# Optimization experiments

Hardware: AMD Instinct MI355X
Metric: run time of the kernel (lower is better)

Reference implementation:

```python
import jax, jax.numpy as jnp
import numpy as np

B, SW, SE, D, H, FF = 8, 512, 128, 1024, 16, 4096
HD = D // H
EPS = 1e-12
SCALE = 1.0 / np.sqrt(HD).astype(np.float32)


def _split_heads(x):
    # [B, S, D] -> [B, H, S, HD]
    b, s, _ = x.shape
    return x.reshape(b, s, H, HD).transpose(0, 2, 1, 3)


def _layer_norm(x, g, b):
    m = jnp.mean(x, axis=-1, keepdims=True)
    v = jnp.mean(jnp.square(x - m), axis=-1, keepdims=True)
    return g * (x - m) / jnp.sqrt(v + EPS) + b


def setup_inputs() -> dict:
    key = jax.random.key(0)
    ks = iter(jax.random.split(key, 40))
    std = 0.02

    def w(i, o):
        return jax.random.normal(next(ks), (i, o), jnp.float32) * std

    inp = {
        "word_hidden_states": jax.random.normal(next(ks), (B, SW, D), jnp.float32),
        "entity_hidden_states": jax.random.normal(next(ks), (B, SE, D), jnp.float32),
        "word_attention_mask": jnp.zeros((B, SW), jnp.float32),
        "entity_attention_mask": jnp.zeros((B, SE), jnp.float32),
        # entity-aware self attention projections
        "Wq": w(D, D), "bq": jnp.zeros((D,), jnp.float32),
        "Ww2e": w(D, D), "bw2e": jnp.zeros((D,), jnp.float32),
        "We2w": w(D, D), "be2w": jnp.zeros((D,), jnp.float32),
        "We2e": w(D, D), "be2e": jnp.zeros((D,), jnp.float32),
        "Wk": w(D, D), "bk": jnp.zeros((D,), jnp.float32),
        "Wv": w(D, D), "bv": jnp.zeros((D,), jnp.float32),
        # BertSelfOutput
        "Wo": w(D, D), "bo": jnp.zeros((D,), jnp.float32),
        "ln1_g": jnp.ones((D,), jnp.float32), "ln1_b": jnp.zeros((D,), jnp.float32),
        # BertIntermediate / BertOutput
        "Wi": w(D, FF), "bi": jnp.zeros((FF,), jnp.float32),
        "Wout": w(FF, D), "bout": jnp.zeros((D,), jnp.float32),
        "ln2_g": jnp.ones((D,), jnp.float32), "ln2_b": jnp.zeros((D,), jnp.float32),
    }
    return inp


def _layer(wh, eh, wmask, emask, Wq, bq, Ww2e, bw2e, We2w, be2w, We2e, be2e,
           Wk, bk, Wv, bv, Wo, bo, ln1_g, ln1_b, Wi, bi, Wout, bout, ln2_g, ln2_b):
    sw = wh.shape[1]
    hidden = jnp.concatenate([wh, eh], axis=1)              # [B, S, D]
    mask = jnp.concatenate([wmask, emask], axis=-1)[:, None, None, :]  # additive

    q_w2w = _split_heads(wh @ Wq + bq)
    q_w2e = _split_heads(wh @ Ww2e + bw2e)
    q_e2w = _split_heads(eh @ We2w + be2w)
    q_e2e = _split_heads(eh @ We2e + be2e)
    k = _split_heads(hidden @ Wk + bk)                      # [B, H, S, HD]
    kw, ke = k[:, :, :sw, :], k[:, :, sw:, :]

    s_w2w = jnp.einsum("bhqd,bhkd->bhqk", q_w2w, kw)
    s_w2e = jnp.einsum("bhqd,bhkd->bhqk", q_w2e, ke)
    s_e2w = jnp.einsum("bhqd,bhkd->bhqk", q_e2w, kw)
    s_e2e = jnp.einsum("bhqd,bhkd->bhqk", q_e2e, ke)
    word_scores = jnp.concatenate([s_w2w, s_w2e], axis=3)
    ent_scores = jnp.concatenate([s_e2w, s_e2e], axis=3)
    scores = jnp.concatenate([word_scores, ent_scores], axis=2) * SCALE + mask
    probs = jax.nn.softmax(scores, axis=-1)

    v = _split_heads(hidden @ Wv + bv)
    ctx = jnp.einsum("bhqk,bhkd->bhqd", probs, v)
    ctx = ctx.transpose(0, 2, 1, 3).reshape(wh.shape[0], -1, D)  # [B, S, D]

    # BertSelfOutput: dense + residual + LN
    attn_out = _layer_norm(ctx @ Wo + bo + hidden, ln1_g, ln1_b)
    # BertIntermediate + BertOutput
    inter = jax.nn.gelu(attn_out @ Wi + bi, approximate=False)
    out = _layer_norm(inter @ Wout + bout + attn_out, ln2_g, ln2_b)
    return out[:, :sw, :], out[:, sw:, :]


def reference(word_hidden_states, entity_hidden_states, word_attention_mask,
              entity_attention_mask, Wq, bq, Ww2e, bw2e, We2w, be2w, We2e, be2e,
              Wk, bk, Wv, bv, Wo, bo, ln1_g, ln1_b, Wi, bi, Wout, bout,
              ln2_g, ln2_b):
    return _layer(word_hidden_states, entity_hidden_states, word_attention_mask,
                  entity_attention_mask, Wq, bq, Ww2e, bw2e, We2w, be2w, We2e,
                  be2e, Wk, bk, Wv, bv, Wo, bo, ln1_g, ln1_b, Wi, bi, Wout,
                  bout, ln2_g, ln2_b)
```

## Files before the change

kernel.cpp:

```cpp
#include <hip/hip_runtime.h>
#include <hip/hip_bf16.h>
#include <stdint.h>
#include <math.h>

#define DEV __device__ __forceinline__

using bf16 = __hip_bfloat16;
typedef __attribute__((ext_vector_type(8))) short bf16x8;
typedef __attribute__((ext_vector_type(4))) float f32x4;

static constexpr int NB  = 8;
static constexpr int NSW = 512;
static constexpr int NSE = 128;
static constexpr int ND  = 1024;
static constexpr int NH  = 16;
static constexpr int NFF = 4096;
static constexpr int NS  = NSW + NSE;
static constexpr int NHD = 64;

DEV f32x4 mfma16(bf16x8 a, bf16x8 b, f32x4 c){
  return __builtin_amdgcn_mfma_f32_16x16x32_bf16(a, b, c, 0, 0, 0);
}

DEV void gload16(const bf16* g, bf16* l){
  __builtin_amdgcn_global_load_lds((const __attribute__((address_space(1))) void*)g,
                                   (__attribute__((address_space(3))) void*)l,
                                   16, 0, 0);
}

DEV bf16 tobf(float f){ return __float2bfloat16(f); }

union PK4 { bf16 h[4]; short4 s; };

__global__ __launch_bounds__(256) void cast_word_k(const float* __restrict__ wh,
                                                   bf16* __restrict__ hid){
  long i = ((long)blockIdx.x*256 + threadIdx.x)*4;
  float4 v = *reinterpret_cast<const float4*>(wh + i);
  PK4 p; p.h[0]=tobf(v.x); p.h[1]=tobf(v.y); p.h[2]=tobf(v.z); p.h[3]=tobf(v.w);
  long row = i >> 10; int c = (int)(i & 1023);
  int b = (int)(row >> 9), s = (int)(row & 511);
  *reinterpret_cast<short4*>(hid + ((long)(b*NS + s) << 10) + c) = p.s;
}

__global__ __launch_bounds__(256) void cast_ent_k(const float* __restrict__ eh,
                                                  bf16* __restrict__ hid){
  long i = ((long)blockIdx.x*256 + threadIdx.x)*4;
  float4 v = *reinterpret_cast<const float4*>(eh + i);
  PK4 p; p.h[0]=tobf(v.x); p.h[1]=tobf(v.y); p.h[2]=tobf(v.z); p.h[3]=tobf(v.w);
  long row = i >> 10; int c = (int)(i & 1023);
  int b = (int)(row >> 7), s = (int)(row & 127);
  *reinterpret_cast<short4*>(hid + ((long)(b*NS + NSW + s) << 10) + c) = p.s;
}

struct TP7 { const float* src[7]; bf16* dst[7]; };

__global__ void transpose7_k(TP7 tp){
  __shared__ float tile[32][33];
  const float* in = tp.src[blockIdx.z];
  bf16* out = tp.dst[blockIdx.z];
  const int c0 = blockIdx.x*32, r0 = blockIdx.y*32;
  const int tx = threadIdx.x, ty = threadIdx.y;
  #pragma unroll
  for (int i=0;i<4;i++)
    tile[ty + i*8][tx] = in[(long)(r0 + ty + i*8)*1024 + c0 + tx];
  __syncthreads();
  #pragma unroll
  for (int i=0;i<4;i++){
    int rr = ty + i*8;
    out[(long)(c0 + rr)*1024 + r0 + tx] = tobf(tile[tx][rr]);
  }
}

__global__ void transpose_cast_k(const float* __restrict__ in, bf16* __restrict__ out,
                                 int R, int C){
  __shared__ float tile[32][33];
  const int c0 = blockIdx.x*32, r0 = blockIdx.y*32;
  const int tx = threadIdx.x, ty = threadIdx.y;
  #pragma unroll
  for (int i=0;i<4;i++)
    tile[ty + i*8][tx] = in[(long)(r0 + ty + i*8)*C + c0 + tx];
  __syncthreads();
  #pragma unroll
  for (int i=0;i<4;i++){
    int rr = ty + i*8;
    out[(long)(c0 + rr)*R + r0 + tx] = tobf(tile[tx][rr]);
  }
}

__global__ void bias_concat_k(const float* __restrict__ bq, const float* __restrict__ bw2e,
                              const float* __restrict__ be2w, const float* __restrict__ be2e,
                              const float* __restrict__ bk, const float* __restrict__ bv,
                              float* __restrict__ bQw, float* __restrict__ bQe,
                              float* __restrict__ bKV){
  int i = blockIdx.x*256 + threadIdx.x;
  bQw[i] = bq[i];   bQw[1024+i] = bw2e[i];
  bQe[i] = be2w[i]; bQe[1024+i] = be2e[i];
  bKV[i] = bk[i];   bKV[1024+i] = bv[i];
}

template<int NF>
DEV void stA(bf16* reg, const bf16* a0, const bf16* a1, int koff, int tid){
  gload16(a0 + koff, reg + tid*8);
  gload16(a1 + koff, reg + (512 + tid)*8);
}
template<int NF>
DEV void stB(bf16* reg, const bf16* b0, const bf16* b1, int koff, int tid){
  gload16(b0 + koff, reg + tid*8);
  if constexpr (NF == 4) gload16(b1 + koff, reg + (512 + tid)*8);
}

template<int NF>
DEV void g256_core(const bf16* a0, const bf16* a1,
                   const bf16* b0, const bf16* b1,
                   int NT, bf16* lds, f32x4 (&acc)[8][NF],
                   int tid, int wr, int wc, int lane){
  constexpr int AKH  = 8192;
  constexpr int BKH  = NF*2048;
  constexpr int BUFE = 2*AKH + 2*BKH;
  auto Areg = [&](int buf,int kh){ return lds + buf*BUFE + kh*AKH; };
  auto Breg = [&](int buf,int kh){ return lds + buf*BUFE + 2*AKH + kh*BKH; };
  auto gate = [&](bool last){
    if (last){
      asm volatile("s_waitcnt vmcnt(0)" ::: "memory");
    } else if constexpr (NF == 4){
      asm volatile("s_waitcnt vmcnt(4)" ::: "memory");
    } else {
      asm volatile("s_waitcnt vmcnt(3)" ::: "memory");
    }
    __builtin_amdgcn_sched_barrier(0);
    asm volatile("s_barrier" ::: "memory");
    __builtin_amdgcn_sched_barrier(0);
  };
  stA<NF>(Areg(0,0), a0, a1, 0,  tid);
  stB<NF>(Breg(0,0), b0, b1, 0,  tid);
  stA<NF>(Areg(0,1), a0, a1, 32, tid);
  stB<NF>(Breg(0,1), b0, b1, 32, tid);
  int kt = 0;
  for (int t=0; t<NT; ++t){
    const int c = t & 1;
    const bool more = (t+1 < NT);
    const int kn = kt + 64;
    #pragma unroll
    for (int ks=0; ks<2; ++ks){
      gate(!more && ks==1);
      if (more) stA<NF>(Areg(c^1, ks), a0, a1, kn + ks*32, tid);
      const bf16* Ar = Areg(c, ks);
      const bf16* Br = Breg(c, ks);
      bf16x8 bfr[NF], afr[4];
      #pragma unroll
      for (int nf=0; nf<NF; ++nf)
        bfr[nf] = *reinterpret_cast<const bf16x8*>(Br + (((wc*NF+nf)<<6) + lane)*8);
      #pragma unroll
      for (int m=0; m<4; ++m)
        afr[m] = *reinterpret_cast<const bf16x8*>(Ar + (((wr*8+m)<<6) + lane)*8);
      __builtin_amdgcn_s_setprio(1);
      #pragma unroll
      for (int m=0; m<4; ++m)
        #pragma unroll
        for (int nf=0; nf<NF; ++nf)
          acc[m][nf] = mfma16(afr[m], bfr[nf], acc[m][nf]);
      __builtin_amdgcn_s_setprio(0);
      if (more) stB<NF>(Breg(c^1, ks), b0, b1, kn + ks*32, tid);
      #pragma unroll
      for (int m=0; m<4; ++m)
        afr[m] = *reinterpret_cast<const bf16x8*>(Ar + (((wr*8+4+m)<<6) + lane)*8);
      __builtin_amdgcn_s_setprio(1);
      #pragma unroll
      for (int m=0; m<4; ++m)
        #pragma unroll
        for (int nf=0; nf<NF; ++nf)
          acc[4+m][nf] = mfma16(afr[m], bfr[nf], acc[4+m][nf]);
      __builtin_amdgcn_s_setprio(0);
    }
    kt = kn;
  }
}

__global__ __launch_bounds__(512, 2) void proj_k(const bf16* __restrict__ hid,
    const bf16* __restrict__ WqwT, const bf16* __restrict__ WqeT,
    const bf16* __restrict__ WkvT,
    const float* __restrict__ bQw, const float* __restrict__ bQe,
    const float* __restrict__ bKV,
    bf16* __restrict__ Qwb, bf16* __restrict__ Qeb,
    bf16* __restrict__ KVb, bf16* __restrict__ Vt){
  __shared__ __align__(16) bf16 lds[2*(2*8192 + 2*8192)];
  const int tid = threadIdx.x, wid = tid>>6, lane = tid&63;
  const int wr = wid>>2, wc = wid&3, lr = lane&15, lg = lane>>4;
  int wg = blockIdx.x;
  { int xcd = wg & 7, idx = wg >> 3; wg = xcd*40 + idx; }
  const bool isKV = (wg >= 160);
  const int loc = isKV ? wg - 160 : wg;
  const int m0 = (loc >> 3)*256, n0 = (loc & 7)*256;
  const bool word = (m0 < 4096);

  const int la = lane & 15, ksub = (lane>>4)*8;
  auto hidrow = [&](int r)->long{
    if (isKV) return r;
    if (word) return (long)((r>>9)*640 + (r&511));
    int r2 = r - 4096; return (long)((r2>>7)*640 + 512 + (r2&127));
  };
  const bf16* a0 = hid + hidrow(m0 + wid*16 + la)*1024 + ksub;
  const bf16* a1 = hid + hidrow(m0 + (wid+8)*16 + la)*1024 + ksub;
  const bf16* Bt = isKV ? WkvT : (word ? WqwT : WqeT);
  const bf16* b0 = Bt + (long)(n0 + wid*16 + la)*1024 + ksub;
  const bf16* b1 = Bt + (long)(n0 + (wid+8)*16 + la)*1024 + ksub;

  f32x4 acc[8][4];
  #pragma unroll
  for (int m=0;m<8;m++)
    #pragma unroll
    for (int n=0;n<4;n++) acc[m][n] = (f32x4){0.f,0.f,0.f,0.f};

  g256_core<4>(a0, a1, b0, b1, 16, lds, acc, tid, wr, wc, lane);

  const float* bias = isKV ? bKV : (word ? bQw : bQe);
  #pragma unroll
  for (int m=0;m<8;m++){
    const int rbase = m0 + wr*128 + m*16 + lg*4;
    #pragma unroll
    for (int nf=0;nf<4;nf++){
      const int col = n0 + wc*64 + nf*16 + lr;
      const float bsv = bias[col];
      #pragma unroll
      for (int r=0;r<4;r++){
        const int rw = rbase + r;
        const float v = acc[m][nf][r] + bsv;
        if (!isKV){
          if (word) Qwb[(long)rw*2048 + col] = tobf(v);
          else      Qeb[(long)(rw-4096)*2048 + col] = tobf(v);
        } else {
          if (col < 1024){
            KVb[(long)rw*2048 + col] = tobf(v);
          } else {
            int b = rw / NS, s = rw % NS, hh = (col-1024)>>6, dd = (col-1024)&63;
            Vt[((long)((b*NH + hh)*NHD + dd))*NS + s] = tobf(v);
          }
        }
      }
    }
  }
}

__global__ __launch_bounds__(512, 2) void ffn1_k(const bf16* __restrict__ A,
    const bf16* __restrict__ Bt, const float* __restrict__ bias,
    bf16* __restrict__ out){
  __shared__ __align__(16) bf16 lds[2*(2*8192 + 2*8192)];
  const int tid = threadIdx.x, wid = tid>>6, lane = tid&63;
  const int wr = wid>>2, wc = wid&3, lr = lane&15, lg = lane>>4;
  int wg = blockIdx.x;
  { int xcd = wg & 7, idx = wg >> 3; wg = xcd*40 + idx; }
  const int m0 = (wg >> 4)*256, n0 = (wg & 15)*256;

  const int la = lane & 15, ksub = (lane>>4)*8;
  const bf16* a0 = A + (long)(m0 + wid*16 + la)*1024 + ksub;
  const bf16* a1 = A + (long)(m0 + (wid+8)*16 + la)*1024 + ksub;
  const bf16* b0 = Bt + (long)(n0 + wid*16 + la)*1024 + ksub;
  const bf16* b1 = Bt + (long)(n0 + (wid+8)*16 + la)*1024 + ksub;

  f32x4 acc[8][4];
  #pragma unroll
  for (int m=0;m<8;m++)
    #pragma unroll
    for (int n=0;n<4;n++) acc[m][n] = (f32x4){0.f,0.f,0.f,0.f};

  g256_core<4>(a0, a1, b0, b1, 16, lds, acc, tid, wr, wc, lane);

  #pragma unroll
  for (int m=0;m<8;m++){
    const int rbase = m0 + wr*128 + m*16 + lg*4;
    #pragma unroll
    for (int nf=0;nf<4;nf++){
      const int col = n0 + wc*64 + nf*16 + lr;
      const float bsv = bias[col];
      #pragma unroll
      for (int r=0;r<4;r++){
        float v = acc[m][nf][r] + bsv;
        float ge = 0.5f*v*(1.0f + erff(v*0.70710678118654752f));
        out[(long)(rbase+r)*NFF + col] = tobf(ge);
      }
    }
  }
}

__global__ __launch_bounds__(512, 2) void ws_k(const bf16* __restrict__ A, int lda,
    const bf16* __restrict__ Bt, const float* __restrict__ bias,
    float* __restrict__ out0, float* __restrict__ out1, int Kc){
  __shared__ __align__(16) bf16 lds[2*(2*8192 + 2*4096)];
  const int tid = threadIdx.x, wid = tid>>6, lane = tid&63;
  const int wr = wid>>2, wc = wid&3, lr = lane&15, lg = lane>>4;
  int wg = blockIdx.x;
  { int xcd = wg & 7, idx = wg >> 3; wg = xcd*20 + idx; }
  const int m0 = (wg >> 3)*256, n0 = (wg & 7)*128;
  const int kt0 = blockIdx.z * Kc;

  const int la = lane & 15, ksub = (lane>>4)*8;
  const bf16* a0 = A + (long)(m0 + wid*16 + la)*lda + kt0 + ksub;
  const bf16* a1 = A + (long)(m0 + (wid+8)*16 + la)*lda + kt0 + ksub;
  const bf16* b0 = Bt + (long)(n0 + wid*16 + la)*lda + kt0 + ksub;

  f32x4 acc[8][2];
  #pragma unroll
  for (int m=0;m<8;m++)
    #pragma unroll
    for (int n=0;n<2;n++) acc[m][n] = (f32x4){0.f,0.f,0.f,0.f};

  g256_core<2>(a0, a1, b0, b0, Kc/64, lds, acc, tid, wr, wc, lane);

  float* out = blockIdx.z ? out1 : out0;
  #pragma unroll
  for (int m=0;m<8;m++){
    const int rbase = m0 + wr*128 + m*16 + lg*4;
    #pragma unroll
    for (int nf=0;nf<2;nf++){
      const int col = n0 + wc*32 + nf*16 + lr;
      const float bsv = blockIdx.z ? 0.f : bias[col];
      #pragma unroll
      for (int r=0;r<4;r++)
        out[(long)(rbase+r)*1024 + col] = acc[m][nf][r] + bsv;
    }
  }
}

__global__ __launch_bounds__(256) void attn_k(
    const bf16* __restrict__ Qw, const bf16* __restrict__ Qe,
    const bf16* __restrict__ KV, const bf16* __restrict__ Vt,
    const float* __restrict__ wm, const float* __restrict__ em,
    bf16* __restrict__ ctx){
  __shared__ __align__(16) bf16 Plds[4][2][16*40];
  __shared__ float mred[4][2][16];
  __shared__ float lred[4][2][16];
  __shared__ __align__(16) float accred[4][16][64];
  const int tid = threadIdx.x, wid = tid>>6, lane = tid&63;
  const int lr = lane&15, lg = lane>>4;
  const int w   = blockIdx.x;
  const int b   = w / (NH*20);
  const int rem = w % (NH*20);
  const int h   = rem / 20;
  const int q0  = (rem % 20)*32;

  const bf16* Qbase; long qrow0;
  if (q0 < NSW){ Qbase = Qw; qrow0 = (long)b*NSW + q0; }
  else         { Qbase = Qe; qrow0 = (long)b*NSE + (q0 - NSW); }

  bf16x8 qA[2][2], qB[2][2];
  #pragma unroll
  for (int m=0;m<2;m++)
    #pragma unroll
    for (int dc=0; dc<2; dc++){
      long o = (qrow0 + m*16 + lr)*2048 + h*NHD + dc*32 + lg*8;
      qA[m][dc] = *reinterpret_cast<const bf16x8*>(Qbase + o);
      qB[m][dc] = *reinterpret_cast<const bf16x8*>(Qbase + o + 1024);
    }

  const f32x4 zero = {0.f,0.f,0.f,0.f};
  f32x4 cacc[2][4];
  float mrow[2][4], lsum[2][4];
  #pragma unroll
  for (int m=0;m<2;m++){
    #pragma unroll
    for (int dt=0;dt<4;dt++) cacc[m][dt] = zero;
    #pragma unroll
    for (int r=0;r<4;r++){ mrow[m][r] = -1e30f; lsum[m][r] = 0.f; }
  }

  const bf16* Kbase = KV + (long)b*NS*2048 + h*NHD;
  const bf16* Vbase = Vt + (long)((b*NH + h)*NHD)*NS;

  for (int kt=wid*5; kt<wid*5+5; kt++){
    const int k0 = kt*32;
    const bool word = (k0 < NSW);

    bf16x8 kf[2][2], vf[4];
    #pragma unroll
    for (int sub=0;sub<2;sub++)
      #pragma unroll
      for (int dc=0;dc<2;dc++)
        kf[sub][dc] = *reinterpret_cast<const bf16x8*>(
            Kbase + (long)(k0 + sub*16 + lr)*2048 + dc*32 + lg*8);
    #pragma unroll
    for (int dt=0;dt<4;dt++)
      vf[dt] = *reinterpret_cast<const bf16x8*>(
          Vbase + (long)(dt*16 + lr)*NS + k0 + lg*8);

    float msk0, msk1;
    { int k = k0 + lr;
      msk0 = word ? wm[b*NSW + k]      : em[b*NSE + (k - NSW)];
      msk1 = word ? wm[b*NSW + k + 16] : em[b*NSE + (k + 16 - NSW)];
    }

    f32x4 sc[2][2];
    #pragma unroll
    for (int m=0;m<2;m++){ sc[m][0]=zero; sc[m][1]=zero; }
    __builtin_amdgcn_s_setprio(1);
    #pragma unroll
    for (int m=0;m<2;m++)
      #pragma unroll
      for (int sub=0;sub<2;sub++)
        #pragma unroll
        for (int dc=0;dc<2;dc++){
          const bf16x8 q = word ? qA[m][dc] : qB[m][dc];
          sc[m][sub] = mfma16(q, kf[sub][dc], sc[m][sub]);
        }
    __builtin_amdgcn_s_setprio(0);

    #pragma unroll
    for (int m=0;m<2;m++){
      bf16* pw = &Plds[wid][m][0];
      #pragma unroll
      for (int r=0;r<4;r++){
        float s0 = sc[m][0][r]*0.125f + msk0;
        float s1 = sc[m][1][r]*0.125f + msk1;
        float t = fmaxf(s0, s1);
        #pragma unroll
        for (int o=8;o;o>>=1) t = fmaxf(t, __shfl_xor(t, o, 16));
        float mn = fmaxf(mrow[m][r], t);
        float al = __expf(mrow[m][r] - mn);
        mrow[m][r] = mn;
        float p0 = __expf(s0 - mn), p1 = __expf(s1 - mn);
        float ps = p0 + p1;
        #pragma unroll
        for (int o=8;o;o>>=1) ps += __shfl_xor(ps, o, 16);
        lsum[m][r] = lsum[m][r]*al + ps;
        pw[(lg*4+r)*40 + lr]      = tobf(p0);
        pw[(lg*4+r)*40 + 16 + lr] = tobf(p1);
        #pragma unroll
        for (int dt=0;dt<4;dt++) cacc[m][dt][r] *= al;
      }
    }

    __builtin_amdgcn_s_setprio(1);
    #pragma unroll
    for (int m=0;m<2;m++){
      bf16x8 pa = *reinterpret_cast<const bf16x8*>(&Plds[wid][m][0] + lr*40 + lg*8);
      #pragma unroll
      for (int dt=0;dt<4;dt++)
        cacc[m][dt] = mfma16(pa, vf[dt], cacc[m][dt]);
    }
    __builtin_amdgcn_s_setprio(0);
  }

  #pragma unroll
  for (int m=0;m<2;m++)
    #pragma unroll
    for (int r=0;r<4;r++)
      if (lr == 0){
        mred[wid][m][lg*4+r] = mrow[m][r];
        lred[wid][m][lg*4+r] = lsum[m][r];
      }
  __syncthreads();

  float Lg[2][4], scl[2][4];
  #pragma unroll
  for (int m=0;m<2;m++)
    #pragma unroll
    for (int r=0;r<4;r++){
      const int row = lg*4 + r;
      float M0 = fmaxf(fmaxf(mred[0][m][row], mred[1][m][row]),
                       fmaxf(mred[2][m][row], mred[3][m][row]));
      float lt = 0.f;
      #pragma unroll
      for (int ww=0; ww<4; ww++)
        lt += lred[ww][m][row] * __expf(mred[ww][m][row] - M0);
      Lg[m][r]  = lt;
      scl[m][r] = __expf(mrow[m][r] - M0);
    }

  const long crow = (long)b*NS + q0;
  #pragma unroll
  for (int m=0;m<2;m++){
    #pragma unroll
    for (int dt=0;dt<4;dt++)
      #pragma unroll
      for (int r=0;r<4;r++)
        accred[wid][dt*4+r][lane] = cacc[m][dt][r] * scl[m][r];
    __syncthreads();
    { const int dt = wid;
      #pragma unroll
      for (int r=0;r<4;r++){
        float s = accred[0][dt*4+r][lane] + accred[1][dt*4+r][lane]
                + accred[2][dt*4+r][lane] + accred[3][dt*4+r][lane];
        s /= Lg[m][r];
        ctx[(crow + m*16 + lg*4 + r)*ND + h*NHD + dt*16 + lr] = tobf(s);
      }
    }
    __syncthreads();
  }
}

DEV void block_red2(float& s1, float& s2){
  __shared__ float red[8];
  #pragma unroll
  for (int o=32;o;o>>=1){ s1 += __shfl_down(s1,o); s2 += __shfl_down(s2,o); }
  int wid = threadIdx.x>>6, lane = threadIdx.x&63;
  if (lane==0){ red[wid]=s1; red[4+wid]=s2; }
  __syncthreads();
  s1 = red[0]+red[1]+red[2]+red[3];
  s2 = red[4]+red[5]+red[6]+red[7];
}

__global__ __launch_bounds__(256) void ln1_k(const float* __restrict__ ctxO,
    const float* __restrict__ ctxO1,
    const float* __restrict__ wh, const float* __restrict__ eh,
    const float* __restrict__ g, const float* __restrict__ be,
    float* __restrict__ outF, bf16* __restrict__ outB){
  const int row = blockIdx.x;
  const int b = row / NS, s = row % NS;
  const float* resid = (s < NSW) ? wh + ((long)(b*NSW + s))*ND
                                 : eh + ((long)(b*NSE + (s-NSW)))*ND;
  const int t = threadIdx.x;
  float4 xv = reinterpret_cast<const float4*>(ctxO + (long)row*ND)[t];
  float4 x1 = reinterpret_cast<const float4*>(ctxO1 + (long)row*ND)[t];
  float4 rv = reinterpret_cast<const float4*>(resid)[t];
  float4 x = make_float4(xv.x+x1.x+rv.x, xv.y+x1.y+rv.y, xv.z+x1.z+rv.z, xv.w+x1.w+rv.w);
  float s1 = x.x+x.y+x.z+x.w;
  float s2 = x.x*x.x + x.y*x.y + x.z*x.z + x.w*x.w;
  block_red2(s1, s2);
  float mean = s1 * (1.f/ND);
  float var  = s2 * (1.f/ND) - mean*mean;
  float rstd = rsqrtf(var + 1e-12f);
  float4 gv = reinterpret_cast<const float4*>(g)[t];
  float4 bv = reinterpret_cast<const float4*>(be)[t];
  float4 y = make_float4(gv.x*(x.x-mean)*rstd + bv.x,
                         gv.y*(x.y-mean)*rstd + bv.y,
                         gv.z*(x.z-mean)*rstd + bv.z,
                         gv.w*(x.w-mean)*rstd + bv.w);
  reinterpret_cast<float4*>(outF + (long)row*ND)[t] = y;
  PK4 p; p.h[0]=tobf(y.x); p.h[1]=tobf(y.y); p.h[2]=tobf(y.z); p.h[3]=tobf(y.w);
  reinterpret_cast<short4*>(outB + (long)row*ND)[t] = p.s;
}

__global__ __launch_bounds__(256) void ln2_k(const float* __restrict__ ffo,
    const float* __restrict__ ffo1,
    const float* __restrict__ attnF, const float* __restrict__ g,
    const float* __restrict__ be, float* __restrict__ out){
  const int row = blockIdx.x;
  const int b = row / NS, s = row % NS;
  const int t = threadIdx.x;
  float4 xv = reinterpret_cast<const float4*>(ffo + (long)row*ND)[t];
  float4 x1 = reinterpret_cast<const float4*>(ffo1 + (long)row*ND)[t];
  float4 rv = reinterpret_cast<const float4*>(attnF + (long)row*ND)[t];
  float4 x = make_float4(xv.x+x1.x+rv.x, xv.y+x1.y+rv.y, xv.z+x1.z+rv.z, xv.w+x1.w+rv.w);
  float s1 = x.x+x.y+x.z+x.w;
  float s2 = x.x*x.x + x.y*x.y + x.z*x.z + x.w*x.w;
  block_red2(s1, s2);
  float mean = s1 * (1.f/ND);
  float var  = s2 * (1.f/ND) - mean*mean;
  float rstd = rsqrtf(var + 1e-12f);
  float4 gv = reinterpret_cast<const float4*>(g)[t];
  float4 bv = reinterpret_cast<const float4*>(be)[t];
  float4 y = make_float4(gv.x*(x.x-mean)*rstd + bv.x,
                         gv.y*(x.y-mean)*rstd + bv.y,
                         gv.z*(x.z-mean)*rstd + bv.z,
                         gv.w*(x.w-mean)*rstd + bv.w);
  float* op = (s < NSW) ? out + ((long)(b*NSW+s))*ND
                        : out + (long)NB*NSW*ND + ((long)(b*NSE + (s-NSW)))*ND;
  reinterpret_cast<float4*>(op)[t] = y;
}

extern "C" void kernel_launch(void* const* d_in, const int* in_sizes, int n_in,
                              void* d_out, int out_size, void* d_ws, size_t ws_size,
                              hipStream_t stream){
  (void)in_sizes; (void)n_in; (void)out_size; (void)ws_size;
  const float* wh   = (const float*)d_in[0];
  const float* eh   = (const float*)d_in[1];
  const float* wm   = (const float*)d_in[2];
  const float* em   = (const float*)d_in[3];
  const float* Wq   = (const float*)d_in[4];   const float* bq   = (const float*)d_in[5];
  const float* Ww2e = (const float*)d_in[6];   const float* bw2e = (const float*)d_in[7];
  const float* We2w = (const float*)d_in[8];   const float* be2w = (const float*)d_in[9];
  const float* We2e = (const float*)d_in[10];  const float* be2e = (const float*)d_in[11];
  const float* Wk   = (const float*)d_in[12];  const float* bk   = (const float*)d_in[13];
  const float* Wv   = (const float*)d_in[14];  const float* bv   = (const float*)d_in[15];
  const float* Wo   = (const float*)d_in[16];  const float* bo   = (const float*)d_in[17];
  const float* g1   = (const float*)d_in[18];  const float* b1   = (const float*)d_in[19];
  const float* Wi   = (const float*)d_in[20];  const float* bi   = (const float*)d_in[21];
  const float* Wout = (const float*)d_in[22];  const float* bout = (const float*)d_in[23];
  const float* g2   = (const float*)d_in[24];  const float* b2   = (const float*)d_in[25];
  float* out = (float*)d_out;

  char* ws = (char*)d_ws;
  size_t off = 0;
  auto alloc = [&](size_t bytes)->char*{
    char* p = ws + off; off += (bytes + 255) & ~(size_t)255; return p;
  };

  bf16* hid   = (bf16*)alloc((size_t)NB*NS*ND*2);
  bf16* WqwT  = (bf16*)alloc((size_t)2048*ND*2);
  bf16* WqeT  = (bf16*)alloc((size_t)2048*ND*2);
  bf16* WkvT  = (bf16*)alloc((size_t)2048*ND*2);
  float* part1 = (float*)hid;
  bf16* WoT   = (bf16*)alloc((size_t)ND*ND*2);
  bf16* WiT   = (bf16*)alloc((size_t)NFF*ND*2);
  bf16* WoutT = (bf16*)alloc((size_t)ND*NFF*2);
  float* bQw  = (float*)alloc(2048*4);
  float* bQe  = (float*)alloc(2048*4);
  float* bKV  = (float*)alloc(2048*4);

  char* u1 = alloc((size_t)52428800);
  bf16* Qwb = (bf16*)u1;
  bf16* Qeb = Qwb + (size_t)NB*NSW*2048;
  bf16* KVb = Qeb + (size_t)NB*NSE*2048;
  bf16* Vt  = KVb + (size_t)NB*NS*2048;
  bf16* inter = (bf16*)u1;
  bf16* attnB = (bf16*)(u1 + (size_t)41943040);

  bf16*  ctx   = (bf16*)alloc((size_t)NB*NS*ND*2);
  float* ctxO  = (float*)alloc((size_t)NB*NS*ND*4);
  float* ffo   = ctxO;
  float* attnF = (float*)alloc((size_t)NB*NS*ND*4);

  dim3 tb(32,8);
  cast_word_k<<<4096, 256, 0, stream>>>(wh, hid);
  cast_ent_k <<<1024, 256, 0, stream>>>(eh, hid);

  TP7 tp;
  tp.src[0]=Wq;   tp.dst[0]=WqwT;
  tp.src[1]=Ww2e; tp.dst[1]=WqwT + (size_t)1024*1024;
  tp.src[2]=We2w; tp.dst[2]=WqeT;
  tp.src[3]=We2e; tp.dst[3]=WqeT + (size_t)1024*1024;
  tp.src[4]=Wk;   tp.dst[4]=WkvT;
  tp.src[5]=Wv;   tp.dst[5]=WkvT + (size_t)1024*1024;
  tp.src[6]=Wo;   tp.dst[6]=WoT;
  transpose7_k<<<dim3(32,32,7), tb, 0, stream>>>(tp);
  transpose_cast_k<<<dim3(128,32), tb, 0, stream>>>(Wi,   WiT,   ND, NFF);
  transpose_cast_k<<<dim3(32,128), tb, 0, stream>>>(Wout, WoutT, NFF, ND);
  bias_concat_k<<<4, 256, 0, stream>>>(bq, bw2e, be2w, be2e, bk, bv, bQw, bQe, bKV);

  proj_k<<<320, 512, 0, stream>>>(hid, WqwT, WqeT, WkvT, bQw, bQe, bKV,
                                  Qwb, Qeb, KVb, Vt);

  attn_k<<<2560, 256, 0, stream>>>(Qwb, Qeb, KVb, Vt, wm, em, ctx);

  ws_k<<<dim3(160,1,2), 512, 0, stream>>>(ctx, 1024, WoT, bo, ctxO, part1, 512);
  ln1_k<<<5120, 256, 0, stream>>>(ctxO, part1, wh, eh, g1, b1, attnF, attnB);
  ffn1_k<<<320, 512, 0, stream>>>(attnB, WiT, bi, inter);
  ws_k<<<dim3(160,1,2), 512, 0, stream>>>(inter, 4096, WoutT, bout, ffo, part1, 2048);
  ln2_k<<<5120, 256, 0, stream>>>(ffo, part1, attnF, g2, b2, out);
}
```

Baseline: 633.1 us.

## Replace double-buffered GEMM k-loop with 4-stage prefetch ring

The shared GEMM core now uses a 4-slot LDS ring of 32-wide k-stages with three stages in flight, instead of double buffering 64-wide k-tiles split into two halves. vmcnt waits are tuned to the number of loads still outstanding, and each stage issues its A and B loads together. The intent is deeper latency hiding of global-to-LDS loads behind MFMA work. LDS per block stays the same size, so occupancy should be unchanged, but more loads are outstanding and the vmcnt accounting becomes more fragile.

```diff
diff --git a/kernel.cpp b/kernel.cpp
--- a/kernel.cpp
+++ b/kernel.cpp
@@ -99,80 +99,67 @@
 }
 
 template<int NF>
-DEV void stA(bf16* reg, const bf16* a0, const bf16* a1, int koff, int tid){
-  gload16(a0 + koff, reg + tid*8);
-  gload16(a1 + koff, reg + (512 + tid)*8);
-}
-template<int NF>
-DEV void stB(bf16* reg, const bf16* b0, const bf16* b1, int koff, int tid){
-  gload16(b0 + koff, reg + tid*8);
-  if constexpr (NF == 4) gload16(b1 + koff, reg + (512 + tid)*8);
+DEV void stage_issue(bf16* buf, const bf16* a0, const bf16* a1,
+                     const bf16* b0, const bf16* b1, int koff, int tid){
+  gload16(a0 + koff, buf + tid*8);
+  gload16(a1 + koff, buf + (512 + tid)*8);
+  gload16(b0 + koff, buf + (1024 + tid)*8);
+  if constexpr (NF == 4) gload16(b1 + koff, buf + (1536 + tid)*8);
 }
 
 template<int NF>
 DEV void g256_core(const bf16* a0, const bf16* a1,
                    const bf16* b0, const bf16* b1,
-                   int NT, bf16* lds, f32x4 (&acc)[8][NF],
+                   int NSs, bf16* lds, f32x4 (&acc)[8][NF],
                    int tid, int wr, int wc, int lane){
-  constexpr int AKH  = 8192;
-  constexpr int BKH  = NF*2048;
-  constexpr int BUFE = 2*AKH + 2*BKH;
-  auto Areg = [&](int buf,int kh){ return lds + buf*BUFE + kh*AKH; };
-  auto Breg = [&](int buf,int kh){ return lds + buf*BUFE + 2*AKH + kh*BKH; };
-  auto gate = [&](bool last){
-    if (last){
-      asm volatile("s_waitcnt vmcnt(0)" ::: "memory");
-    } else if constexpr (NF == 4){
-      asm volatile("s_waitcnt vmcnt(4)" ::: "memory");
-    } else {
-      asm volatile("s_waitcnt vmcnt(3)" ::: "memory");
-    }
+  constexpr int BUFE = (1024 + NF*256)*8;
+  constexpr int LPS  = (NF == 4) ? 4 : 3;
+  auto buf = [&](int s){ return lds + (s & 3)*BUFE; };
+
+  stage_issue<NF>(buf(0), a0,a1,b0,b1, 0,  tid);
+  stage_issue<NF>(buf(1), a0,a1,b0,b1, 32, tid);
+  stage_issue<NF>(buf(2), a0,a1,b0,b1, 64, tid);
+
+  for (int s=0; s<NSs; ++s){
+    const int r = NSs - 1 - s;
+    const int pend = (r >= 2 ? 2 : r) * LPS;
+    if      (pend == 8) asm volatile("s_waitcnt vmcnt(8)" ::: "memory");
+    else if (pend == 6) asm volatile("s_waitcnt vmcnt(6)" ::: "memory");
+    else if (pend == 4) asm volatile("s_waitcnt vmcnt(4)" ::: "memory");
+    else if (pend == 3) asm volatile("s_waitcnt vmcnt(3)" ::: "memory");
+    else                asm volatile("s_waitcnt vmcnt(0)" ::: "memory");
     __builtin_amdgcn_sched_barrier(0);
     asm volatile("s_barrier" ::: "memory");
     __builtin_amdgcn_sched_barrier(0);
-  };
-  stA<NF>(Areg(0,0), a0, a1, 0,  tid);
-  stB<NF>(Breg(0,0), b0, b1, 0,  tid);
-  stA<NF>(Areg(0,1), a0, a1, 32, tid);
-  stB<NF>(Breg(0,1), b0, b1, 32, tid);
-  int kt = 0;
-  for (int t=0; t<NT; ++t){
-    const int c = t & 1;
-    const bool more = (t+1 < NT);
-    const int kn = kt + 64;
-    #pragma unroll
-    for (int ks=0; ks<2; ++ks){
-      gate(!more && ks==1);
-      if (more) stA<NF>(Areg(c^1, ks), a0, a1, kn + ks*32, tid);
-      const bf16* Ar = Areg(c, ks);
-      const bf16* Br = Breg(c, ks);
-      bf16x8 bfr[NF], afr[4];
+
+    if (s+3 < NSs) stage_issue<NF>(buf(s+3), a0,a1,b0,b1, (s+3)*32, tid);
+
+    const bf16* Ar = buf(s);
+    const bf16* Br = buf(s) + 1024*8;
+    bf16x8 bfr[NF], afr[4];
+    #pragma unroll
+    for (int nf=0; nf<NF; ++nf)
+      bfr[nf] = *reinterpret_cast<const bf16x8*>(Br + (((wc*NF+nf)<<6) + lane)*8);
+    #pragma unroll
+    for (int m=0; m<4; ++m)
+      afr[m] = *reinterpret_cast<const bf16x8*>(Ar + (((wr*8+m)<<6) + lane)*8);
+    __builtin_amdgcn_s_setprio(1);
+    #pragma unroll
+    for (int m=0; m<4; ++m)
       #pragma unroll
       for (int nf=0; nf<NF; ++nf)
-        bfr[nf] = *reinterpret_cast<const bf16x8*>(Br + (((wc*NF+nf)<<6) + lane)*8);
-      #pragma unroll
-      for (int m=0; m<4; ++m)
-        afr[m] = *reinterpret_cast<const bf16x8*>(Ar + (((wr*8+m)<<6) + lane)*8);
-      __builtin_amdgcn_s_setprio(1);
-      #pragma unroll
-      for (int m=0; m<4; ++m)
-        #pragma unroll
-        for (int nf=0; nf<NF; ++nf)
-          acc[m][nf] = mfma16(afr[m], bfr[nf], acc[m][nf]);
-      __builtin_amdgcn_s_setprio(0);
-      if (more) stB<NF>(Breg(c^1, ks), b0, b1, kn + ks*32, tid);
-      #pragma unroll
-      for (int m=0; m<4; ++m)
-        afr[m] = *reinterpret_cast<const bf16x8*>(Ar + (((wr*8+4+m)<<6) + lane)*8);
-      __builtin_amdgcn_s_setprio(1);
-      #pragma unroll
-      for (int m=0; m<4; ++m)
-        #pragma unroll
-        for (int nf=0; nf<NF; ++nf)
-          acc[4+m][nf] = mfma16(afr[m], bfr[nf], acc[4+m][nf]);
-      __builtin_amdgcn_s_setprio(0);
-    }
-    kt = kn;
+        acc[m][nf] = mfma16(afr[m], bfr[nf], acc[m][nf]);
+    __builtin_amdgcn_s_setprio(0);
+    #pragma unroll
+    for (int m=0; m<4; ++m)
+      afr[m] = *reinterpret_cast<const bf16x8*>(Ar + (((wr*8+4+m)<<6) + lane)*8);
+    __builtin_amdgcn_s_setprio(1);
+    #pragma unroll
+    for (int m=0; m<4; ++m)
+      #pragma unroll
+      for (int nf=0; nf<NF; ++nf)
+        acc[4+m][nf] = mfma16(afr[m], bfr[nf], acc[4+m][nf]);
+    __builtin_amdgcn_s_setprio(0);
   }
 }
 
@@ -183,7 +170,7 @@
     const float* __restrict__ bKV,
     bf16* __restrict__ Qwb, bf16* __restrict__ Qeb,
     bf16* __restrict__ KVb, bf16* __restrict__ Vt){
-  __shared__ __align__(16) bf16 lds[2*(2*8192 + 2*8192)];
+  __shared__ __align__(16) bf16 lds[4*16384];
   const int tid = threadIdx.x, wid = tid>>6, lane = tid&63;
   const int wr = wid>>2, wc = wid&3, lr = lane&15, lg = lane>>4;
   int wg = blockIdx.x;
@@ -211,7 +198,7 @@
     #pragma unroll
     for (int n=0;n<4;n++) acc[m][n] = (f32x4){0.f,0.f,0.f,0.f};
 
-  g256_core<4>(a0, a1, b0, b1, 16, lds, acc, tid, wr, wc, lane);
+  g256_core<4>(a0, a1, b0, b1, 32, lds, acc, tid, wr, wc, lane);
 
   const float* bias = isKV ? bKV : (word ? bQw : bQe);
   #pragma unroll
@@ -244,7 +231,7 @@
 __global__ __launch_bounds__(512, 2) void ffn1_k(const bf16* __restrict__ A,
     const bf16* __restrict__ Bt, const float* __restrict__ bias,
     bf16* __restrict__ out){
-  __shared__ __align__(16) bf16 lds[2*(2*8192 + 2*8192)];
+  __shared__ __align__(16) bf16 lds[4*16384];
   const int tid = threadIdx.x, wid = tid>>6, lane = tid&63;
   const int wr = wid>>2, wc = wid&3, lr = lane&15, lg = lane>>4;
   int wg = blockIdx.x;
@@ -263,7 +250,7 @@
     #pragma unroll
     for (int n=0;n<4;n++) acc[m][n] = (f32x4){0.f,0.f,0.f,0.f};
 
-  g256_core<4>(a0, a1, b0, b1, 16, lds, acc, tid, wr, wc, lane);
+  g256_core<4>(a0, a1, b0, b1, 32, lds, acc, tid, wr, wc, lane);
 
   #pragma unroll
   for (int m=0;m<8;m++){
@@ -285,7 +272,7 @@
 __global__ __launch_bounds__(512, 2) void ws_k(const bf16* __restrict__ A, int lda,
     const bf16* __restrict__ Bt, const float* __restrict__ bias,
     float* __restrict__ out0, float* __restrict__ out1, int Kc){
-  __shared__ __align__(16) bf16 lds[2*(2*8192 + 2*4096)];
+  __shared__ __align__(16) bf16 lds[4*12288];
   const int tid = threadIdx.x, wid = tid>>6, lane = tid&63;
   const int wr = wid>>2, wc = wid&3, lr = lane&15, lg = lane>>4;
   int wg = blockIdx.x;
@@ -304,7 +291,7 @@
     #pragma unroll
     for (int n=0;n<2;n++) acc[m][n] = (f32x4){0.f,0.f,0.f,0.f};
 
-  g256_core<2>(a0, a1, b0, b0, Kc/64, lds, acc, tid, wr, wc, lane);
+  g256_core<2>(a0, a1, b0, b0, Kc/32, lds, acc, tid, wr, wc, lane);
 
   float* out = blockIdx.z ? out1 : out0;
   #pragma unroll
```

Result: no change. 635.9 us (+0.4%).
